# Performance work log

Measured on AMD Instinct MI355X. Metric: run time of the kernel, lower is better.

Reference implementation:

```python
import jax, jax.numpy as jnp
import numpy as np

EPS = 1e-6
DELTA = 1e-6
GAMMA = 1.0


def setup_inputs() -> dict:
    key = jax.random.key(0)
    ks = jax.random.split(key, 6)
    B, N, D, DDIR, DSIM = 2, 384, 256, 128, 64
    sc = lambda d: 1.0 / np.sqrt(d)
    return {
        "t": jax.random.normal(ks[0], (B, N, D), jnp.float32),
        "Qd": jax.random.normal(ks[1], (D, DDIR), jnp.float32) * sc(D),
        "Kd": jax.random.normal(ks[2], (D, DDIR), jnp.float32) * sc(D),
        "Vd": jax.random.normal(ks[3], (DDIR, D), jnp.float32) * sc(DDIR),
        "Qs": jax.random.normal(ks[4], (D, DSIM), jnp.float32) * sc(D),
        "Ks": jax.random.normal(ks[5], (D, DSIM), jnp.float32) * sc(D),
        "a_l": jnp.ones((1,), jnp.float32),
        "b_l": jnp.zeros((1,), jnp.float32),
    }


def reference(t, Qd, Kd, Vd, Qs, Ks, a_l, b_l):
    B, N, D = t.shape
    d_sim = Qs.shape[1]
    # --- similarity: s_ij = <Qs t_i, Ks t_j>/sqrt(d_sim), then symmetrize ---
    q = t @ Qs  # (B,N,d_sim)
    k = t @ Ks
    s = jnp.einsum('bnd,bmd->bnm', q, k) / jnp.sqrt(jnp.float32(d_sim))
    s = 0.5 * (s + s.transpose(0, 2, 1))
    # --- global z-score over off-diagonal entries (biased var) ---
    eye = jnp.eye(N, dtype=bool)[None]  # (1,N,N)
    cnt = jnp.float32(N * (N - 1))
    mu = jnp.where(eye, 0.0, s).sum((1, 2), keepdims=True) / cnt  # (B,1,1)
    var = jnp.where(eye, 0.0, (s - mu) ** 2).sum((1, 2), keepdims=True) / cnt
    s_hat = (s - mu) / jnp.sqrt(var + EPS)
    tilde_s = a_l.reshape(-1, 1, 1) * s_hat + b_l.reshape(-1, 1, 1)
    # --- gates / mass / inertia / apportioned step ---
    A = jax.nn.sigmoid(tilde_s)                                  # (B,N,N)
    m = 1.0 / (jnp.exp(GAMMA * tilde_s).sum(axis=2) + EPS)       # (B,N)
    w = A * m[:, None, :]                                        # w_ij = m_j A_ij
    alpha = A * (w / (w.sum(axis=2, keepdims=True) + DELTA))     # (B,N,N)
    # --- antisymmetric Hadamard direction gate ---
    qd = t @ Qd  # (B,N,d_dir)
    kd = t @ Kd
    had = qd[:, :, None, :] * kd[:, None, :, :]                  # (B,N,N,d_dir)
    kappa = jnp.einsum('bijr,rd->bijd', had, Vd)                 # (B,N,N,D)
    gate = jax.nn.sigmoid(kappa - kappa.transpose(0, 2, 1, 3))
    Dpair = gate * (t[:, :, None, :] - t[:, None, :, :])         # D_ij = gate*(t_i - t_j)
    # --- exclude self pairs, aggregate update ---
    off = ~eye  # (1,N,N)
    alpha = jnp.where(off, alpha, 0.0)
    Dpair = jnp.where(off[..., None], Dpair, 0.0)
    t_next = t - jnp.einsum('bnm,bnmd->bnd', alpha, Dpair)
    return t_next
```

## Files before the change

### kernel.cpp

```cpp
#include <hip/hip_runtime.h>

#define Bn 2
#define Nn 384
#define Dn 256
#define Rn 128
#define Sn 64
#define BNn (Bn*Nn)
#define JT 64
#define NEG_LOG2E -1.44269504088896f

typedef short short8 __attribute__((ext_vector_type(8)));
typedef float f32x4 __attribute__((ext_vector_type(4)));
typedef unsigned int uint;
typedef unsigned short ushort;

static __device__ __forceinline__ float fast_sigmoid(float x) {
    return __builtin_amdgcn_rcpf(1.0f + __expf(-x));
}
static __device__ __forceinline__ ushort f2bf(float f) {
    uint u = __float_as_uint(f);
    uint r = (u + 0x7fffu + ((u >> 16) & 1u)) >> 16;
    return (ushort)r;
}
static __device__ __forceinline__ float bf2f(ushort u) {
    return __uint_as_float(((uint)u) << 16);
}

__global__ __launch_bounds__(256)
void prep_kernel(const float* __restrict__ t,
                 const float* __restrict__ Qd, const float* __restrict__ Kd,
                 const float* __restrict__ Vd,
                 const float* __restrict__ Qs, const float* __restrict__ Ks,
                 float* __restrict__ q, float* __restrict__ k,
                 ushort* __restrict__ qdb, ushort* __restrict__ kdb,
                 ushort* __restrict__ VdT, float* __restrict__ stats) {
    const int bi = blockIdx.x;
    const int tid = threadIdx.x;
    if (bi >= 192) {
        const int idx = (bi - 192) * 256 + tid;
        const int d = idx >> 7, r = idx & 127;
        VdT[idx] = f2bf(NEG_LOG2E * Vd[(size_t)r * Dn + d]);
        if (bi == 319 && tid < 4) stats[tid] = 0.0f;
        return;
    }
    __shared__ float trow[4][Dn];
    const int r0 = bi * 4;
    for (int idx = tid; idx < 4 * Dn; idx += 256)
        trow[idx >> 8][idx & 255] = t[(size_t)r0 * Dn + idx];
    __syncthreads();
    {
        const float* W = (tid < 128) ? Qd : Kd;
        ushort* ob = (tid < 128) ? qdb : kdb;
        const int col = tid & 127;
        float a0 = 0.f, a1 = 0.f, a2 = 0.f, a3 = 0.f;
        for (int kk = 0; kk < Dn; kk += 4) {
            float4 t0 = *(const float4*)&trow[0][kk];
            float4 t1 = *(const float4*)&trow[1][kk];
            float4 t2 = *(const float4*)&trow[2][kk];
            float4 t3 = *(const float4*)&trow[3][kk];
            float w0 = W[(size_t)(kk + 0) * 128 + col];
            float w1 = W[(size_t)(kk + 1) * 128 + col];
            float w2 = W[(size_t)(kk + 2) * 128 + col];
            float w3 = W[(size_t)(kk + 3) * 128 + col];
            a0 += t0.x * w0 + t0.y * w1 + t0.z * w2 + t0.w * w3;
            a1 += t1.x * w0 + t1.y * w1 + t1.z * w2 + t1.w * w3;
            a2 += t2.x * w0 + t2.y * w1 + t2.z * w2 + t2.w * w3;
            a3 += t3.x * w0 + t3.y * w1 + t3.z * w2 + t3.w * w3;
        }
        ob[(size_t)(r0 + 0) * 128 + col] = f2bf(a0);
        ob[(size_t)(r0 + 1) * 128 + col] = f2bf(a1);
        ob[(size_t)(r0 + 2) * 128 + col] = f2bf(a2);
        ob[(size_t)(r0 + 3) * 128 + col] = f2bf(a3);
    }
    if (tid < 128) {
        const float* W = (tid < 64) ? Qs : Ks;
        float* of = (tid < 64) ? q : k;
        const int col = tid & 63;
        float a0 = 0.f, a1 = 0.f, a2 = 0.f, a3 = 0.f;
        for (int kk = 0; kk < Dn; kk += 4) {
            float4 t0 = *(const float4*)&trow[0][kk];
            float4 t1 = *(const float4*)&trow[1][kk];
            float4 t2 = *(const float4*)&trow[2][kk];
            float4 t3 = *(const float4*)&trow[3][kk];
            float w0 = W[(size_t)(kk + 0) * 64 + col];
            float w1 = W[(size_t)(kk + 1) * 64 + col];
            float w2 = W[(size_t)(kk + 2) * 64 + col];
            float w3 = W[(size_t)(kk + 3) * 64 + col];
            a0 += t0.x * w0 + t0.y * w1 + t0.z * w2 + t0.w * w3;
            a1 += t1.x * w0 + t1.y * w1 + t1.z * w2 + t1.w * w3;
            a2 += t2.x * w0 + t2.y * w1 + t2.z * w2 + t2.w * w3;
            a3 += t3.x * w0 + t3.y * w1 + t3.z * w2 + t3.w * w3;
        }
        of[(size_t)(r0 + 0) * 64 + col] = a0;
        of[(size_t)(r0 + 1) * 64 + col] = a1;
        of[(size_t)(r0 + 2) * 64 + col] = a2;
        of[(size_t)(r0 + 3) * 64 + col] = a3;
    }
}

__global__ __launch_bounds__(256)
void ssym_kernel(const float* __restrict__ q, const float* __restrict__ k,
                 float* __restrict__ ssym, float* __restrict__ stats) {
    __shared__ float qi[16][68], ki[16][68], qj[16][68], kj[16][68];
    __shared__ float part[8];
    const int b = blockIdx.z, it = blockIdx.x, jt = blockIdx.y;
    const int tid = threadIdx.x;
    const int r0 = tid >> 6, c = tid & 63;
#pragma unroll
    for (int p = 0; p < 4; ++p) {
        int row = r0 + 4 * p;
        qi[row][c] = q[((size_t)(b * Nn + it * 16 + row)) * Sn + c];
        ki[row][c] = k[((size_t)(b * Nn + it * 16 + row)) * Sn + c];
        qj[row][c] = q[((size_t)(b * Nn + jt * 16 + row)) * Sn + c];
        kj[row][c] = k[((size_t)(b * Nn + jt * 16 + row)) * Sn + c];
    }
    __syncthreads();
    const int ti = tid >> 4, tj = tid & 15;
    float acc = 0.0f;
#pragma unroll
    for (int dd = 0; dd < Sn; dd += 4) {
        float4 a  = *(const float4*)&qi[ti][dd];
        float4 bb = *(const float4*)&kj[tj][dd];
        float4 cc = *(const float4*)&qj[tj][dd];
        float4 d  = *(const float4*)&ki[ti][dd];
        acc += a.x * bb.x + a.y * bb.y + a.z * bb.z + a.w * bb.w
             + cc.x * d.x + cc.y * d.y + cc.z * d.z + cc.w * d.w;
    }
    const float sval = acc * 0.0625f;
    const int gi = it * 16 + ti, gj = jt * 16 + tj;
    ssym[((size_t)(b * Nn + gi)) * Nn + gj] = sval;
    const float v = (gi == gj) ? 0.0f : sval;

    float vs = v, v2 = v * v;
#pragma unroll
    for (int mask = 32; mask > 0; mask >>= 1) {
        vs += __shfl_xor(vs, mask);
        v2 += __shfl_xor(v2, mask);
    }
    const int lane = tid & 63, wave = tid >> 6;
    if (lane == 0) { part[wave] = vs; part[4 + wave] = v2; }
    __syncthreads();
    if (tid == 0) {
        atomicAdd(&stats[b * 2 + 0], part[0] + part[1] + part[2] + part[3]);
        atomicAdd(&stats[b * 2 + 1], part[4] + part[5] + part[6] + part[7]);
    }
}

__global__ __launch_bounds__(256)
void m_kernel(const float* __restrict__ ssym, const float* __restrict__ stats,
              const float* __restrict__ a_l, const float* __restrict__ b_l,
              float* __restrict__ m) {
    __shared__ float part[4];
    const int row = blockIdx.x;
    const int b = row / Nn;
    const float cnt_inv = 1.0f / (float)(Nn * (Nn - 1));
    const float mu = stats[b * 2 + 0] * cnt_inv;
    const float var = stats[b * 2 + 1] * cnt_inv - mu * mu;
    const float isg = rsqrtf(var + 1e-6f);
    const float a = a_l[0], bbias = b_l[0];
    const int tid = threadIdx.x;
    float sum = __expf(a * (ssym[(size_t)row * Nn + tid] - mu) * isg + bbias);
    if (tid < 128)
        sum += __expf(a * (ssym[(size_t)row * Nn + 256 + tid] - mu) * isg + bbias);
#pragma unroll
    for (int mask = 32; mask > 0; mask >>= 1) sum += __shfl_xor(sum, mask);
    if ((tid & 63) == 0) part[tid >> 6] = sum;
    __syncthreads();
    if (tid == 0) m[row] = 1.0f / (part[0] + part[1] + part[2] + part[3] + 1e-6f);
}

__global__ __launch_bounds__(256)
void alpha_kernel(const float* __restrict__ ssym, const float* __restrict__ stats,
                  const float* __restrict__ mptr,
                  const float* __restrict__ a_l, const float* __restrict__ b_l,
                  float* __restrict__ alpha) {
    __shared__ float part[4];
    const int row = blockIdx.x;
    const int b = row / Nn;
    const int i = row - b * Nn;
    const float cnt_inv = 1.0f / (float)(Nn * (Nn - 1));
    const float mu = stats[b * 2 + 0] * cnt_inv;
    const float var = stats[b * 2 + 1] * cnt_inv - mu * mu;
    const float isg = rsqrtf(var + 1e-6f);
    const float a = a_l[0], bbias = b_l[0];
    const int tid = threadIdx.x;
    float A0, am0, A1 = 0.f, am1 = 0.f;
    {
        float s0 = ssym[(size_t)row * Nn + tid];
        A0 = fast_sigmoid(a * (s0 - mu) * isg + bbias);
        am0 = A0 * mptr[b * Nn + tid];
    }
    if (tid < 128) {
        float s1 = ssym[(size_t)row * Nn + 256 + tid];
        A1 = fast_sigmoid(a * (s1 - mu) * isg + bbias);
        am1 = A1 * mptr[b * Nn + 256 + tid];
    }
    float sum = am0 + am1;
#pragma unroll
    for (int mask = 32; mask > 0; mask >>= 1) sum += __shfl_xor(sum, mask);
    if ((tid & 63) == 0) part[tid >> 6] = sum;
    __syncthreads();
    const float inv = 1.0f / (part[0] + part[1] + part[2] + part[3] + 1e-6f);
    alpha[(size_t)row * Nn + tid] = (tid == i) ? 0.f : A0 * am0 * inv;
    if (tid < 128)
        alpha[(size_t)row * Nn + 256 + tid] = ((256 + tid) == i) ? 0.f : A1 * am1 * inv;
}

__global__ __launch_bounds__(256, 4)
void pair_kernel(const float* __restrict__ t, const float* __restrict__ alpha,
                 const ushort* __restrict__ qdb, const ushort* __restrict__ kdb,
                 const ushort* __restrict__ VdT, float* __restrict__ out) {
    __shared__ ushort h_s[JT][136];
    __shared__ float qdi_s[Rn], kdi_s[Rn];

    const int blk = blockIdx.x;
    const int bi = blk >> 1;
    const int dh = blk & 1;
    const int b = bi / Nn;
    const int tid = threadIdx.x;
    const int wave = tid >> 6, lane = tid & 63;
    const int ln = lane & 15, quad = lane >> 4;
    const int wd0 = dh * 128 + wave * 32;

    if (tid < Rn) {
        qdi_s[tid] = bf2f(qdb[(size_t)bi * Rn + tid]);
        kdi_s[tid] = bf2f(kdb[(size_t)bi * Rn + tid]);
    }

    short8 vf[2][4];
#pragma unroll
    for (int dt = 0; dt < 2; ++dt)
#pragma unroll
        for (int ks = 0; ks < 4; ++ks)
            vf[dt][ks] = *(const short8*)&VdT[(size_t)(wd0 + dt * 16 + ln) * Rn + ks * 32 + quad * 8];

    float4 tiv[2];
#pragma unroll
    for (int dt = 0; dt < 2; ++dt)
        tiv[dt] = *(const float4*)&t[(size_t)bi * Dn + wd0 + dt * 16 + quad * 4];

    float4 outac[2];
#pragma unroll
    for (int dt = 0; dt < 2; ++dt) outac[dt] = make_float4(0.f, 0.f, 0.f, 0.f);

    const float* alpr = alpha + (size_t)bi * Nn;

    for (int jt0 = 0; jt0 < Nn; jt0 += JT) {
        __syncthreads();
        {
            const int jj = tid >> 2;
            const int r0s = (tid & 3) * 32;
            const size_t rowj = (size_t)(b * Nn + jt0 + jj) * Rn;
            const uint4* qp = (const uint4*)(qdb + rowj + r0s);
            const uint4* kp = (const uint4*)(kdb + rowj + r0s);
#pragma unroll
            for (int c = 0; c < 4; ++c) {
                uint4 qv = qp[c], kv = kp[c];
                uint pk[4];
#pragma unroll
                for (int p = 0; p < 4; ++p) {
                    uint qu = (&qv.x)[p], ku = (&kv.x)[p];
                    float qlo = __uint_as_float(qu << 16);
                    float qhi = __uint_as_float(qu & 0xffff0000u);
                    float klo = __uint_as_float(ku << 16);
                    float khi = __uint_as_float(ku & 0xffff0000u);
                    const int r = r0s + c * 8 + p * 2;
                    float h0 = qdi_s[r]     * klo - kdi_s[r]     * qlo;
                    float h1 = qdi_s[r + 1] * khi - kdi_s[r + 1] * qhi;
                    pk[p] = (uint)f2bf(h0) | ((uint)f2bf(h1) << 16);
                }
                uint4 w; w.x = pk[0]; w.y = pk[1]; w.z = pk[2]; w.w = pk[3];
                *(uint4*)&h_s[jj][r0s + c * 8] = w;
            }
        }
        __syncthreads();

#pragma unroll 1
        for (int jsub = 0; jsub < 4; ++jsub) {
            short8 hf[4];
#pragma unroll
            for (int ks = 0; ks < 4; ++ks)
                hf[ks] = *(const short8*)&h_s[jsub * 16 + ln][ks * 32 + quad * 8];
            const int j = jt0 + jsub * 16 + ln;
            const float al = alpr[j];
            const size_t trow_ = (size_t)(b * Nn + j) * Dn;
            float4 tjv[2];
#pragma unroll
            for (int dt = 0; dt < 2; ++dt)
                tjv[dt] = *(const float4*)&t[trow_ + wd0 + dt * 16 + quad * 4];

            f32x4 aA[2], aB[2];
#pragma unroll
            for (int dt = 0; dt < 2; ++dt) {
                f32x4 x = {0.f, 0.f, 0.f, 0.f}, y = {0.f, 0.f, 0.f, 0.f};
                x = __builtin_amdgcn_mfma_f32_16x16x32_bf16(vf[dt][0], hf[0], x, 0, 0, 0);
                y = __builtin_amdgcn_mfma_f32_16x16x32_bf16(vf[dt][1], hf[1], y, 0, 0, 0);
                x = __builtin_amdgcn_mfma_f32_16x16x32_bf16(vf[dt][2], hf[2], x, 0, 0, 0);
                y = __builtin_amdgcn_mfma_f32_16x16x32_bf16(vf[dt][3], hf[3], y, 0, 0, 0);
                aA[dt] = x; aB[dt] = y;
            }
#pragma unroll
            for (int dt = 0; dt < 2; ++dt) {
                const float4 tj = tjv[dt];
                float e0 = aA[dt][0] + aB[dt][0];
                float e1 = aA[dt][1] + aB[dt][1];
                float e2 = aA[dt][2] + aB[dt][2];
                float e3 = aA[dt][3] + aB[dt][3];
                float g0 = __builtin_amdgcn_rcpf(1.0f + __builtin_amdgcn_exp2f(e0));
                float g1 = __builtin_amdgcn_rcpf(1.0f + __builtin_amdgcn_exp2f(e1));
                float g2 = __builtin_amdgcn_rcpf(1.0f + __builtin_amdgcn_exp2f(e2));
                float g3 = __builtin_amdgcn_rcpf(1.0f + __builtin_amdgcn_exp2f(e3));
                outac[dt].x += al * g0 * (tiv[dt].x - tj.x);
                outac[dt].y += al * g1 * (tiv[dt].y - tj.y);
                outac[dt].z += al * g2 * (tiv[dt].z - tj.z);
                outac[dt].w += al * g3 * (tiv[dt].w - tj.w);
            }
        }
    }

#pragma unroll
    for (int dt = 0; dt < 2; ++dt) {
        float4 v = outac[dt];
#pragma unroll
        for (int mask = 1; mask < 16; mask <<= 1) {
            v.x += __shfl_xor(v.x, mask);
            v.y += __shfl_xor(v.y, mask);
            v.z += __shfl_xor(v.z, mask);
            v.w += __shfl_xor(v.w, mask);
        }
        if (ln == 0) {
            float4 o;
            o.x = tiv[dt].x - v.x;
            o.y = tiv[dt].y - v.y;
            o.z = tiv[dt].z - v.z;
            o.w = tiv[dt].w - v.w;
            *(float4*)&out[(size_t)bi * Dn + wd0 + dt * 16 + quad * 4] = o;
        }
    }
}

extern "C" void kernel_launch(void* const* d_in, const int* in_sizes, int n_in,
                              void* d_out, int out_size, void* d_ws, size_t ws_size,
                              hipStream_t stream) {
    const float* t   = (const float*)d_in[0];
    const float* Qd  = (const float*)d_in[1];
    const float* Kd  = (const float*)d_in[2];
    const float* Vd  = (const float*)d_in[3];
    const float* Qs  = (const float*)d_in[4];
    const float* Ks  = (const float*)d_in[5];
    const float* a_l = (const float*)d_in[6];
    const float* b_l = (const float*)d_in[7];
    float* out = (float*)d_out;
    float* ws  = (float*)d_ws;

    float* q     = ws;
    float* k     = q + BNn * Sn;
    float* ssym  = k + BNn * Sn;
    float* m     = ssym + (size_t)BNn * Nn;
    float* stats = m + BNn;
    ushort* qdb  = (ushort*)(stats + 8);
    ushort* kdb  = qdb + (size_t)BNn * Rn;
    ushort* VdT  = kdb + (size_t)BNn * Rn;
    float* alpha = (float*)(VdT + (size_t)Dn * Rn);

    hipLaunchKernelGGL(prep_kernel, dim3(320), dim3(256), 0, stream,
                       t, Qd, Kd, Vd, Qs, Ks, q, k, qdb, kdb, VdT, stats);
    hipLaunchKernelGGL(ssym_kernel, dim3(Nn / 16, Nn / 16, Bn), dim3(256), 0, stream,
                       q, k, ssym, stats);
    hipLaunchKernelGGL(m_kernel, dim3(BNn), dim3(256), 0, stream, ssym, stats, a_l, b_l, m);
    hipLaunchKernelGGL(alpha_kernel, dim3(BNn), dim3(256), 0, stream,
                       ssym, stats, m, a_l, b_l, alpha);
    hipLaunchKernelGGL(pair_kernel, dim3(BNn * 2), dim3(256), 0, stream,
                       t, alpha, qdb, kdb, VdT, out);
}
```

Before: 185.3 us.

## Factor Hadamard gate via per-row Vd scaling, fuse alpha into pair kernel

The pair kernel no longer builds the antisymmetric Hadamard matrix in shared memory for each j tile. It instead pre-scales Vd by qd_i and kd_i once per row, giving U and W, and computes kappa_ij - kappa_ji as U·kd_j - W·qd_j with twice the MFMAs, reading qd/kd rows directly from global memory. The alpha kernel is fused into the pair kernel's prologue, which removes a launch and the alpha buffer round trip. prep_kernel now handles one row per block instead of four. The trade is more MFMA work, extra bf16 rounding of the products, and less weight reuse in prep.

```diff
diff --git a/kernel.cpp b/kernel.cpp
--- a/kernel.cpp
+++ b/kernel.cpp
@@ -6,7 +6,6 @@
 #define Rn 128
 #define Sn 64
 #define BNn (Bn*Nn)
-#define JT 64
 #define NEG_LOG2E -1.44269504088896f
 
 typedef short short8 __attribute__((ext_vector_type(8)));
@@ -36,65 +35,43 @@
                  ushort* __restrict__ VdT, float* __restrict__ stats) {
     const int bi = blockIdx.x;
     const int tid = threadIdx.x;
-    if (bi >= 192) {
-        const int idx = (bi - 192) * 256 + tid;
+    if (bi >= BNn) {
+        const int idx = (bi - BNn) * 256 + tid;
         const int d = idx >> 7, r = idx & 127;
         VdT[idx] = f2bf(NEG_LOG2E * Vd[(size_t)r * Dn + d]);
-        if (bi == 319 && tid < 4) stats[tid] = 0.0f;
+        if (bi == BNn && tid < 4) stats[tid] = 0.0f;
         return;
     }
-    __shared__ float trow[4][Dn];
-    const int r0 = bi * 4;
-    for (int idx = tid; idx < 4 * Dn; idx += 256)
-        trow[idx >> 8][idx & 255] = t[(size_t)r0 * Dn + idx];
+    __shared__ float trow[Dn];
+    trow[tid] = t[(size_t)bi * Dn + tid];
     __syncthreads();
     {
         const float* W = (tid < 128) ? Qd : Kd;
         ushort* ob = (tid < 128) ? qdb : kdb;
         const int col = tid & 127;
-        float a0 = 0.f, a1 = 0.f, a2 = 0.f, a3 = 0.f;
+        float a0 = 0.f;
         for (int kk = 0; kk < Dn; kk += 4) {
-            float4 t0 = *(const float4*)&trow[0][kk];
-            float4 t1 = *(const float4*)&trow[1][kk];
-            float4 t2 = *(const float4*)&trow[2][kk];
-            float4 t3 = *(const float4*)&trow[3][kk];
-            float w0 = W[(size_t)(kk + 0) * 128 + col];
-            float w1 = W[(size_t)(kk + 1) * 128 + col];
-            float w2 = W[(size_t)(kk + 2) * 128 + col];
-            float w3 = W[(size_t)(kk + 3) * 128 + col];
-            a0 += t0.x * w0 + t0.y * w1 + t0.z * w2 + t0.w * w3;
-            a1 += t1.x * w0 + t1.y * w1 + t1.z * w2 + t1.w * w3;
-            a2 += t2.x * w0 + t2.y * w1 + t2.z * w2 + t2.w * w3;
-            a3 += t3.x * w0 + t3.y * w1 + t3.z * w2 + t3.w * w3;
-        }
-        ob[(size_t)(r0 + 0) * 128 + col] = f2bf(a0);
-        ob[(size_t)(r0 + 1) * 128 + col] = f2bf(a1);
-        ob[(size_t)(r0 + 2) * 128 + col] = f2bf(a2);
-        ob[(size_t)(r0 + 3) * 128 + col] = f2bf(a3);
+            float4 tv = *(const float4*)&trow[kk];
+            a0 += tv.x * W[(size_t)(kk + 0) * 128 + col]
+                + tv.y * W[(size_t)(kk + 1) * 128 + col]
+                + tv.z * W[(size_t)(kk + 2) * 128 + col]
+                + tv.w * W[(size_t)(kk + 3) * 128 + col];
+        }
+        ob[(size_t)bi * 128 + col] = f2bf(a0);
     }
     if (tid < 128) {
         const float* W = (tid < 64) ? Qs : Ks;
         float* of = (tid < 64) ? q : k;
         const int col = tid & 63;
-        float a0 = 0.f, a1 = 0.f, a2 = 0.f, a3 = 0.f;
+        float a0 = 0.f;
         for (int kk = 0; kk < Dn; kk += 4) {
-            float4 t0 = *(const float4*)&trow[0][kk];
-            float4 t1 = *(const float4*)&trow[1][kk];
-            float4 t2 = *(const float4*)&trow[2][kk];
-            float4 t3 = *(const float4*)&trow[3][kk];
-            float w0 = W[(size_t)(kk + 0) * 64 + col];
-            float w1 = W[(size_t)(kk + 1) * 64 + col];
-            float w2 = W[(size_t)(kk + 2) * 64 + col];
-            float w3 = W[(size_t)(kk + 3) * 64 + col];
-            a0 += t0.x * w0 + t0.y * w1 + t0.z * w2 + t0.w * w3;
-            a1 += t1.x * w0 + t1.y * w1 + t1.z * w2 + t1.w * w3;
-            a2 += t2.x * w0 + t2.y * w1 + t2.z * w2 + t2.w * w3;
-            a3 += t3.x * w0 + t3.y * w1 + t3.z * w2 + t3.w * w3;
-        }
-        of[(size_t)(r0 + 0) * 64 + col] = a0;
-        of[(size_t)(r0 + 1) * 64 + col] = a1;
-        of[(size_t)(r0 + 2) * 64 + col] = a2;
-        of[(size_t)(r0 + 3) * 64 + col] = a3;
+            float4 tv = *(const float4*)&trow[kk];
+            a0 += tv.x * W[(size_t)(kk + 0) * 64 + col]
+                + tv.y * W[(size_t)(kk + 1) * 64 + col]
+                + tv.z * W[(size_t)(kk + 2) * 64 + col]
+                + tv.w * W[(size_t)(kk + 3) * 64 + col];
+        }
+        of[(size_t)bi * 64 + col] = a0;
     }
 }
 
@@ -169,70 +146,76 @@
     if (tid == 0) m[row] = 1.0f / (part[0] + part[1] + part[2] + part[3] + 1e-6f);
 }
 
-__global__ __launch_bounds__(256)
-void alpha_kernel(const float* __restrict__ ssym, const float* __restrict__ stats,
-                  const float* __restrict__ mptr,
-                  const float* __restrict__ a_l, const float* __restrict__ b_l,
-                  float* __restrict__ alpha) {
-    __shared__ float part[4];
-    const int row = blockIdx.x;
-    const int b = row / Nn;
-    const int i = row - b * Nn;
-    const float cnt_inv = 1.0f / (float)(Nn * (Nn - 1));
-    const float mu = stats[b * 2 + 0] * cnt_inv;
-    const float var = stats[b * 2 + 1] * cnt_inv - mu * mu;
-    const float isg = rsqrtf(var + 1e-6f);
-    const float a = a_l[0], bbias = b_l[0];
-    const int tid = threadIdx.x;
-    float A0, am0, A1 = 0.f, am1 = 0.f;
-    {
-        float s0 = ssym[(size_t)row * Nn + tid];
-        A0 = fast_sigmoid(a * (s0 - mu) * isg + bbias);
-        am0 = A0 * mptr[b * Nn + tid];
-    }
-    if (tid < 128) {
-        float s1 = ssym[(size_t)row * Nn + 256 + tid];
-        A1 = fast_sigmoid(a * (s1 - mu) * isg + bbias);
-        am1 = A1 * mptr[b * Nn + 256 + tid];
-    }
-    float sum = am0 + am1;
-#pragma unroll
-    for (int mask = 32; mask > 0; mask >>= 1) sum += __shfl_xor(sum, mask);
-    if ((tid & 63) == 0) part[tid >> 6] = sum;
-    __syncthreads();
-    const float inv = 1.0f / (part[0] + part[1] + part[2] + part[3] + 1e-6f);
-    alpha[(size_t)row * Nn + tid] = (tid == i) ? 0.f : A0 * am0 * inv;
-    if (tid < 128)
-        alpha[(size_t)row * Nn + 256 + tid] = ((256 + tid) == i) ? 0.f : A1 * am1 * inv;
-}
-
 __global__ __launch_bounds__(256, 4)
-void pair_kernel(const float* __restrict__ t, const float* __restrict__ alpha,
+void pair_kernel(const float* __restrict__ t, const float* __restrict__ ssym,
+                 const float* __restrict__ mptr, const float* __restrict__ stats,
+                 const float* __restrict__ a_l, const float* __restrict__ b_l,
                  const ushort* __restrict__ qdb, const ushort* __restrict__ kdb,
                  const ushort* __restrict__ VdT, float* __restrict__ out) {
-    __shared__ ushort h_s[JT][136];
-    __shared__ float qdi_s[Rn], kdi_s[Rn];
+    __shared__ float alpha_s[Nn];
+    __shared__ float part[4];
 
     const int blk = blockIdx.x;
     const int bi = blk >> 1;
     const int dh = blk & 1;
     const int b = bi / Nn;
+    const int i = bi - b * Nn;
     const int tid = threadIdx.x;
     const int wave = tid >> 6, lane = tid & 63;
     const int ln = lane & 15, quad = lane >> 4;
     const int wd0 = dh * 128 + wave * 32;
 
-    if (tid < Rn) {
-        qdi_s[tid] = bf2f(qdb[(size_t)bi * Rn + tid]);
-        kdi_s[tid] = bf2f(kdb[(size_t)bi * Rn + tid]);
-    }
-
-    short8 vf[2][4];
-#pragma unroll
-    for (int dt = 0; dt < 2; ++dt)
-#pragma unroll
-        for (int ks = 0; ks < 4; ++ks)
-            vf[dt][ks] = *(const short8*)&VdT[(size_t)(wd0 + dt * 16 + ln) * Rn + ks * 32 + quad * 8];
+    {
+        const float cnt_inv = 1.0f / (float)(Nn * (Nn - 1));
+        const float mu = stats[b * 2 + 0] * cnt_inv;
+        const float var = stats[b * 2 + 1] * cnt_inv - mu * mu;
+        const float isg = rsqrtf(var + 1e-6f);
+        const float a = a_l[0], bbias = b_l[0];
+        float A0, am0, A1 = 0.f, am1 = 0.f;
+        {
+            float s0 = ssym[(size_t)bi * Nn + tid];
+            A0 = fast_sigmoid(a * (s0 - mu) * isg + bbias);
+            am0 = A0 * mptr[b * Nn + tid];
+        }
+        if (tid < 128) {
+            float s1 = ssym[(size_t)bi * Nn + 256 + tid];
+            A1 = fast_sigmoid(a * (s1 - mu) * isg + bbias);
+            am1 = A1 * mptr[b * Nn + 256 + tid];
+        }
+        float sum = am0 + am1;
+#pragma unroll
+        for (int mask = 32; mask > 0; mask >>= 1) sum += __shfl_xor(sum, mask);
+        if (lane == 0) part[wave] = sum;
+        __syncthreads();
+        const float inv = 1.0f / (part[0] + part[1] + part[2] + part[3] + 1e-6f);
+        alpha_s[tid] = (tid == i) ? 0.f : A0 * am0 * inv;
+        if (tid < 128)
+            alpha_s[256 + tid] = ((256 + tid) == i) ? 0.f : A1 * am1 * inv;
+        __syncthreads();
+    }
+
+    short8 uf[2][4], wf[2][4];
+    {
+        const size_t qrow = (size_t)bi * Rn;
+#pragma unroll
+        for (int ks = 0; ks < 4; ++ks) {
+            short8 qv = *(const short8*)&qdb[qrow + ks * 32 + quad * 8];
+            short8 kv = *(const short8*)&kdb[qrow + ks * 32 + quad * 8];
+#pragma unroll
+            for (int dt = 0; dt < 2; ++dt) {
+                short8 vv = *(const short8*)&VdT[(size_t)(wd0 + dt * 16 + ln) * Rn + ks * 32 + quad * 8];
+                short8 uu, ww;
+#pragma unroll
+                for (int e = 0; e < 8; ++e) {
+                    float vf_ = bf2f((ushort)vv[e]);
+                    uu[e] = (short)f2bf(vf_ * bf2f((ushort)qv[e]));
+                    ww[e] = (short)f2bf(vf_ * bf2f((ushort)kv[e]));
+                }
+                uf[dt][ks] = uu;
+                wf[dt][ks] = ww;
+            }
+        }
+    }
 
     float4 tiv[2];
 #pragma unroll
@@ -243,78 +226,57 @@
 #pragma unroll
     for (int dt = 0; dt < 2; ++dt) outac[dt] = make_float4(0.f, 0.f, 0.f, 0.f);
 
-    const float* alpr = alpha + (size_t)bi * Nn;
-
-    for (int jt0 = 0; jt0 < Nn; jt0 += JT) {
-        __syncthreads();
+    const ushort* qbase = qdb + (size_t)b * Nn * Rn;
+    const ushort* kbase = kdb + (size_t)b * Nn * Rn;
+
+#pragma unroll 1
+    for (int jsub = 0; jsub < Nn / 16; ++jsub) {
+        const int j = jsub * 16 + ln;
+        const float al = alpha_s[j];
+        const size_t brow = (size_t)j * Rn + quad * 8;
+
+        f32x4 accU0 = {0.f, 0.f, 0.f, 0.f}, accW0 = {0.f, 0.f, 0.f, 0.f};
+        f32x4 accU1 = {0.f, 0.f, 0.f, 0.f}, accW1 = {0.f, 0.f, 0.f, 0.f};
+#pragma unroll
+        for (int ks = 0; ks < 4; ++ks) {
+            short8 bk = *(const short8*)&kbase[brow + ks * 32];
+            short8 bq = *(const short8*)&qbase[brow + ks * 32];
+            accU0 = __builtin_amdgcn_mfma_f32_16x16x32_bf16(uf[0][ks], bk, accU0, 0, 0, 0);
+            accW0 = __builtin_amdgcn_mfma_f32_16x16x32_bf16(wf[0][ks], bq, accW0, 0, 0, 0);
+            accU1 = __builtin_amdgcn_mfma_f32_16x16x32_bf16(uf[1][ks], bk, accU1, 0, 0, 0);
+            accW1 = __builtin_amdgcn_mfma_f32_16x16x32_bf16(wf[1][ks], bq, accW1, 0, 0, 0);
+        }
+        const size_t trow_ = (size_t)(b * Nn + j) * Dn + wd0 + quad * 4;
+        float4 tj0 = *(const float4*)&t[trow_];
+        float4 tj1 = *(const float4*)&t[trow_ + 16];
+
         {
-            const int jj = tid >> 2;
-            const int r0s = (tid & 3) * 32;
-            const size_t rowj = (size_t)(b * Nn + jt0 + jj) * Rn;
-            const uint4* qp = (const uint4*)(qdb + rowj + r0s);
-            const uint4* kp = (const uint4*)(kdb + rowj + r0s);
-#pragma unroll
-            for (int c = 0; c < 4; ++c) {
-                uint4 qv = qp[c], kv = kp[c];
-                uint pk[4];
-#pragma unroll
-                for (int p = 0; p < 4; ++p) {
-                    uint qu = (&qv.x)[p], ku = (&kv.x)[p];
-                    float qlo = __uint_as_float(qu << 16);
-                    float qhi = __uint_as_float(qu & 0xffff0000u);
-                    float klo = __uint_as_float(ku << 16);
-                    float khi = __uint_as_float(ku & 0xffff0000u);
-                    const int r = r0s + c * 8 + p * 2;
-                    float h0 = qdi_s[r]     * klo - kdi_s[r]     * qlo;
-                    float h1 = qdi_s[r + 1] * khi - kdi_s[r + 1] * qhi;
-                    pk[p] = (uint)f2bf(h0) | ((uint)f2bf(h1) << 16);
-                }
-                uint4 w; w.x = pk[0]; w.y = pk[1]; w.z = pk[2]; w.w = pk[3];
-                *(uint4*)&h_s[jj][r0s + c * 8] = w;
-            }
-        }
-        __syncthreads();
-
-#pragma unroll 1
-        for (int jsub = 0; jsub < 4; ++jsub) {
-            short8 hf[4];
-#pragma unroll
-            for (int ks = 0; ks < 4; ++ks)
-                hf[ks] = *(const short8*)&h_s[jsub * 16 + ln][ks * 32 + quad * 8];
-            const int j = jt0 + jsub * 16 + ln;
-            const float al = alpr[j];
-            const size_t trow_ = (size_t)(b * Nn + j) * Dn;
-            float4 tjv[2];
-#pragma unroll
-            for (int dt = 0; dt < 2; ++dt)
-                tjv[dt] = *(const float4*)&t[trow_ + wd0 + dt * 16 + quad * 4];
-
-            f32x4 aA[2], aB[2];
-#pragma unroll
-            for (int dt = 0; dt < 2; ++dt) {
-                f32x4 x = {0.f, 0.f, 0.f, 0.f}, y = {0.f, 0.f, 0.f, 0.f};
-                x = __builtin_amdgcn_mfma_f32_16x16x32_bf16(vf[dt][0], hf[0], x, 0, 0, 0);
-                y = __builtin_amdgcn_mfma_f32_16x16x32_bf16(vf[dt][1], hf[1], y, 0, 0, 0);
-                x = __builtin_amdgcn_mfma_f32_16x16x32_bf16(vf[dt][2], hf[2], x, 0, 0, 0);
-                y = __builtin_amdgcn_mfma_f32_16x16x32_bf16(vf[dt][3], hf[3], y, 0, 0, 0);
-                aA[dt] = x; aB[dt] = y;
-            }
-#pragma unroll
-            for (int dt = 0; dt < 2; ++dt) {
-                const float4 tj = tjv[dt];
-                float e0 = aA[dt][0] + aB[dt][0];
-                float e1 = aA[dt][1] + aB[dt][1];
-                float e2 = aA[dt][2] + aB[dt][2];
-                float e3 = aA[dt][3] + aB[dt][3];
-                float g0 = __builtin_amdgcn_rcpf(1.0f + __builtin_amdgcn_exp2f(e0));
-                float g1 = __builtin_amdgcn_rcpf(1.0f + __builtin_amdgcn_exp2f(e1));
-                float g2 = __builtin_amdgcn_rcpf(1.0f + __builtin_amdgcn_exp2f(e2));
-                float g3 = __builtin_amdgcn_rcpf(1.0f + __builtin_amdgcn_exp2f(e3));
-                outac[dt].x += al * g0 * (tiv[dt].x - tj.x);
-                outac[dt].y += al * g1 * (tiv[dt].y - tj.y);
-                outac[dt].z += al * g2 * (tiv[dt].z - tj.z);
-                outac[dt].w += al * g3 * (tiv[dt].w - tj.w);
-            }
+            float e0 = accU0[0] - accW0[0];
+            float e1 = accU0[1] - accW0[1];
+            float e2 = accU0[2] - accW0[2];
+            float e3 = accU0[3] - accW0[3];
+            float g0 = __builtin_amdgcn_rcpf(1.0f + __builtin_amdgcn_exp2f(e0));
+            float g1 = __builtin_amdgcn_rcpf(1.0f + __builtin_amdgcn_exp2f(e1));
+            float g2 = __builtin_amdgcn_rcpf(1.0f + __builtin_amdgcn_exp2f(e2));
+            float g3 = __builtin_amdgcn_rcpf(1.0f + __builtin_amdgcn_exp2f(e3));
+            outac[0].x += al * g0 * (tiv[0].x - tj0.x);
+            outac[0].y += al * g1 * (tiv[0].y - tj0.y);
+            outac[0].z += al * g2 * (tiv[0].z - tj0.z);
+            outac[0].w += al * g3 * (tiv[0].w - tj0.w);
+        }
+        {
+            float e0 = accU1[0] - accW1[0];
+            float e1 = accU1[1] - accW1[1];
+            float e2 = accU1[2] - accW1[2];
+            float e3 = accU1[3] - accW1[3];
+            float g0 = __builtin_amdgcn_rcpf(1.0f + __builtin_amdgcn_exp2f(e0));
+            float g1 = __builtin_amdgcn_rcpf(1.0f + __builtin_amdgcn_exp2f(e1));
+            float g2 = __builtin_amdgcn_rcpf(1.0f + __builtin_amdgcn_exp2f(e2));
+            float g3 = __builtin_amdgcn_rcpf(1.0f + __builtin_amdgcn_exp2f(e3));
+            outac[1].x += al * g0 * (tiv[1].x - tj1.x);
+            outac[1].y += al * g1 * (tiv[1].y - tj1.y);
+            outac[1].z += al * g2 * (tiv[1].z - tj1.z);
+            outac[1].w += al * g3 * (tiv[1].w - tj1.w);
         }
     }
 
@@ -361,15 +323,12 @@
     ushort* qdb  = (ushort*)(stats + 8);
     ushort* kdb  = qdb + (size_t)BNn * Rn;
     ushort* VdT  = kdb + (size_t)BNn * Rn;
-    float* alpha = (float*)(VdT + (size_t)Dn * Rn);
-
-    hipLaunchKernelGGL(prep_kernel, dim3(320), dim3(256), 0, stream,
+
+    hipLaunchKernelGGL(prep_kernel, dim3(BNn + 128), dim3(256), 0, stream,
                        t, Qd, Kd, Vd, Qs, Ks, q, k, qdb, kdb, VdT, stats);
     hipLaunchKernelGGL(ssym_kernel, dim3(Nn / 16, Nn / 16, Bn), dim3(256), 0, stream,
                        q, k, ssym, stats);
     hipLaunchKernelGGL(m_kernel, dim3(BNn), dim3(256), 0, stream, ssym, stats, a_l, b_l, m);
-    hipLaunchKernelGGL(alpha_kernel, dim3(BNn), dim3(256), 0, stream,
-                       ssym, stats, m, a_l, b_l, alpha);
     hipLaunchKernelGGL(pair_kernel, dim3(BNn * 2), dim3(256), 0, stream,
-                       t, alpha, qdb, kdb, VdT, out);
-}
+                       t, ssym, m, stats, a_l, b_l, qdb, kdb, VdT, out);
+}
```

Measured after the change: 365.4 us. 1.97x slower.
